# Performance work log

Measured on AMD Instinct MI355X. Metric: run time of the kernel, lower is better.

Reference implementation:

```python
import jax, jax.numpy as jnp
import numpy as np

B, C, F_IN, F_OUT = 2048, 63, 250, 250
NEG_SLOPE = 0.2
N = B * C  # flattened node count


def _build_edge_index():
    # fixed fully-connected (no self) graph over the FIRST 63 nodes only
    src = np.array([i for i in range(C) for j in range(C) if i != j], dtype=np.int32)
    dst = np.array([j for i in range(C) for j in range(C) if i != j], dtype=np.int32)
    # PyG GATConv add_self_loops=True: self loop for every node (num_nodes = N)
    loops = np.arange(N, dtype=np.int32)
    src = np.concatenate([src, loops])
    dst = np.concatenate([dst, loops])
    return jnp.asarray(np.stack([src, dst]))  # [2, E]


def setup_inputs() -> dict:
    key = jax.random.key(0)
    kx, kw, ks, kd = jax.random.split(key, 4)
    x = jax.random.normal(kx, (B, 1, C, F_IN), dtype=jnp.float32)
    # GATConv params (heads=1): lin weight, att_src, att_dst, bias
    W = jax.random.normal(kw, (F_IN, F_OUT), dtype=jnp.float32) / np.sqrt(F_IN)
    att_src = jax.random.normal(ks, (F_OUT,), dtype=jnp.float32) / np.sqrt(F_OUT)
    att_dst = jax.random.normal(kd, (F_OUT,), dtype=jnp.float32) / np.sqrt(F_OUT)
    bias = jnp.zeros((F_OUT,), dtype=jnp.float32)
    return {"x": x, "W": W, "att_src": att_src, "att_dst": att_dst,
            "bias": bias, "edge_index": _build_edge_index()}


def reference(x, W, att_src, att_dst, bias, edge_index):
    b, _, c, f = x.shape
    n = b * c
    h = x.reshape(n, f) @ W                      # [N, F_OUT]
    a_src = h @ att_src                          # [N]
    a_dst = h @ att_dst                          # [N]
    src, dst = edge_index[0], edge_index[1]
    e = jax.nn.leaky_relu(a_src[src] + a_dst[dst], NEG_SLOPE)  # [E]
    # segment softmax over incoming edges of each dst node (stable)
    m = jax.ops.segment_max(e, dst, num_segments=n)
    ex = jnp.exp(e - m[dst])
    denom = jax.ops.segment_sum(ex, dst, num_segments=n)
    alpha = ex / denom[dst]                      # [E]
    out = jax.ops.segment_sum(alpha[:, None] * h[src], dst, num_segments=n)
    out = out + bias
    return out.reshape(b, 1, c, -1)              # [B,1,63,F_OUT]
```

## Files before the change

kernel.cpp:

```cpp
#include <hip/hip_runtime.h>
#include <cstdint>
#include <cstddef>

#define M_TOTAL 129024
#define KDIM    250
#define NDIM    250
#define BM      32
#define TPB     8
#define NBLK    504
#define TILE_F  (BM*KDIM)
#define LDSF    8008

typedef float  f32x4  __attribute__((ext_vector_type(4)));
typedef float  f32x2  __attribute__((ext_vector_type(2)));
typedef __bf16 bf16x8 __attribute__((ext_vector_type(8)));

static __device__ __forceinline__ unsigned short f2bf(float f) {
  unsigned u = __float_as_uint(f);
  u += 0x7fffu + ((u >> 16) & 1u);
  return (unsigned short)(u >> 16);
}

static __device__ __forceinline__ float wsum(float v) {
#pragma unroll
  for (int o = 32; o > 0; o >>= 1) v += __shfl_xor(v, o, 64);
  return v;
}
static __device__ __forceinline__ float wmaxr(float v) {
#pragma unroll
  for (int o = 32; o > 0; o >>= 1) v = fmaxf(v, __shfl_xor(v, o, 64));
  return v;
}

static __device__ __forceinline__ void gll16(const float* g, float* l) {
  __builtin_amdgcn_global_load_lds(
      (const __attribute__((address_space(1))) void*)g,
      (__attribute__((address_space(3))) void*)l, 16, 0, 0);
}
static __device__ __forceinline__ void gll4(const float* g, float* l) {
  __builtin_amdgcn_global_load_lds(
      (const __attribute__((address_space(1))) void*)g,
      (__attribute__((address_space(3))) void*)l, 4, 0, 0);
}

__global__ void wcvt_kernel(const float* __restrict__ W, unsigned short* __restrict__ WTf) {
  const int f     = blockIdx.x * 256 + threadIdx.x;
  const int lane  = f & 63;
  const int kk    = (f >> 6) & 7;
  const int ntile = f >> 9;
  const int n     = ntile * 16 + (lane & 15);
  const int k0    = kk * 32 + (lane >> 4) * 8;
  unsigned u[4];
#pragma unroll
  for (int p = 0; p < 4; ++p) {
    const int ka = k0 + 2 * p, kb = k0 + 2 * p + 1;
    unsigned short a = (n < NDIM && ka < KDIM) ? f2bf(W[(size_t)ka * NDIM + n]) : 0;
    unsigned short b = (n < NDIM && kb < KDIM) ? f2bf(W[(size_t)kb * NDIM + n]) : 0;
    u[p] = (unsigned)a | ((unsigned)b << 16);
  }
  *reinterpret_cast<uint4*>(WTf + (size_t)f * 8) = make_uint4(u[0], u[1], u[2], u[3]);
}

__global__ __launch_bounds__(256, 2) void gemm_kernel(
    const float* __restrict__ X, const unsigned short* __restrict__ WTf,
    const float* __restrict__ bias, float* __restrict__ out,
    float* __restrict__ h63) {
  __shared__ __attribute__((aligned(16))) float lX[2 * LDSF];

  const int tid  = threadIdx.x;
  const int lane = tid & 63;
  const int w    = tid >> 6;
  const int r16  = lane & 15;
  const int quad = lane >> 4;

  if (tid < 8) { lX[TILE_F + tid] = 0.f; lX[LDSF + TILE_F + tid] = 0.f; }

  bf16x8 wf[4][8];
#pragma unroll
  for (int ft = 0; ft < 4; ++ft)
#pragma unroll
    for (int kk = 0; kk < 8; ++kk)
      wf[ft][kk] = *reinterpret_cast<const bf16x8*>(
          WTf + (size_t)((((w * 4 + ft) * 8) + kk) * 64 + lane) * 8);

  float bv[4][4];
#pragma unroll
  for (int ft = 0; ft < 4; ++ft)
#pragma unroll
    for (int i = 0; i < 4; ++i) {
      const int c = w * 64 + ft * 16 + quad * 4 + i;
      bv[ft][i] = (c < NDIM) ? bias[c] : 0.f;
    }

  const int tile0 = blockIdx.x * TPB;

  auto stage = [&](int buf, int g) {
    const float* gb = X + (size_t)g * TILE_F;
    float* lb = &lX[buf * LDSF];
    if (w < 3) {
#pragma unroll
      for (int c = 0; c < 8; ++c) {
        const int ch = w * 8 + c;
        gll16(gb + ch * 256 + lane * 4, lb + ch * 256);
      }
    } else {
#pragma unroll
      for (int c = 0; c < 7; ++c) {
        const int ch = 24 + c;
        gll16(gb + ch * 256 + lane * 4, lb + ch * 256);
      }
      gll4(gb + 7936 + lane, lb + 7936);
    }
  };

  stage(0, tile0);

  for (int t = 0; t < TPB; ++t) {
    const int cur = t & 1;
    __syncthreads();
    if (t + 1 < TPB) stage(cur ^ 1, tile0 + t + 1);

    const float* Bp = &lX[cur * LDSF];
    f32x4 acc[4][2];
#pragma unroll
    for (int ft = 0; ft < 4; ++ft)
#pragma unroll
      for (int nt = 0; nt < 2; ++nt) acc[ft][nt] = f32x4{0.f, 0.f, 0.f, 0.f};

#pragma unroll
    for (int kk = 0; kk < 8; ++kk) {
      bf16x8 xf[2];
#pragma unroll
      for (int nt = 0; nt < 2; ++nt) {
        const float* p = Bp + (size_t)(nt * 16 + r16) * KDIM + kk * 32 + quad * 8;
        const f32x2 a = *reinterpret_cast<const f32x2*>(p);
        const f32x2 b = *reinterpret_cast<const f32x2*>(p + 2);
        const f32x2 c = *reinterpret_cast<const f32x2*>(p + 4);
        const f32x2 d = *reinterpret_cast<const f32x2*>(p + 6);
        bf16x8 v;
        v[0] = (__bf16)a.x; v[1] = (__bf16)a.y;
        v[2] = (__bf16)b.x; v[3] = (__bf16)b.y;
        v[4] = (__bf16)c.x; v[5] = (__bf16)c.y;
        v[6] = (__bf16)d.x; v[7] = (__bf16)d.y;
        xf[nt] = v;
      }
#pragma unroll
      for (int ft = 0; ft < 4; ++ft)
#pragma unroll
        for (int nt = 0; nt < 2; ++nt)
          acc[ft][nt] = __builtin_amdgcn_mfma_f32_16x16x32_bf16(
              wf[ft][kk], xf[nt], acc[ft][nt], 0, 0, 0);
    }

    const int rbase = (tile0 + t) * BM;
#pragma unroll
    for (int ft = 0; ft < 4; ++ft) {
      const int c0 = w * 64 + ft * 16 + quad * 4;
#pragma unroll
      for (int nt = 0; nt < 2; ++nt) {
        const int row = rbase + nt * 16 + r16;
        float* o = out + (size_t)row * NDIM + c0;
        const f32x4 a = acc[ft][nt];
        if (c0 + 1 < NDIM) {
          f32x2 s = {a.x + bv[ft][0], a.y + bv[ft][1]};
          *reinterpret_cast<f32x2*>(o) = s;
        }
        if (c0 + 3 < NDIM) {
          f32x2 s = {a.z + bv[ft][2], a.w + bv[ft][3]};
          *reinterpret_cast<f32x2*>(o + 2) = s;
        }
      }
    }
    if (rbase < 63) {
#pragma unroll
      for (int ft = 0; ft < 4; ++ft) {
        const int c0 = w * 64 + ft * 16 + quad * 4;
#pragma unroll
        for (int nt = 0; nt < 2; ++nt) {
          const int row = rbase + nt * 16 + r16;
          if (row < 63) {
            const f32x4 a = acc[ft][nt];
#pragma unroll
            for (int i = 0; i < 4; ++i)
              if (c0 + i < NDIM) h63[(size_t)row * NDIM + c0 + i] = a[i];
          }
        }
      }
    }
  }
}

__global__ void att_kernel(const float* __restrict__ h, const float* __restrict__ att_src,
                           const float* __restrict__ att_dst, const float* __restrict__ bias,
                           float* __restrict__ out) {
  const int d = blockIdx.x;
  const int tid = threadIdx.x;
  const int lane = tid & 63;
  const int wid = tid >> 6;

  __shared__ float s_asrc[64];
  __shared__ float s_adst;
  __shared__ float s_alpha[64];

  for (int s = wid; s < 63; s += 4) {
    float sum = 0.f;
    for (int f = lane; f < NDIM; f += 64) sum += h[s * NDIM + f] * att_src[f];
    sum = wsum(sum);
    if (lane == 0) s_asrc[s] = sum;
  }
  if (wid == 0) {
    float sum = 0.f;
    for (int f = lane; f < NDIM; f += 64) sum += h[d * NDIM + f] * att_dst[f];
    sum = wsum(sum);
    if (lane == 0) s_adst = sum;
  }
  __syncthreads();

  if (wid == 0) {
    float e = -__builtin_inff();
    if (lane < 63) {
      float x = s_asrc[lane] + s_adst;
      e = (x > 0.f) ? x : 0.2f * x;
    }
    const float m = wmaxr(e);
    const float p = (lane < 63) ? expf(e - m) : 0.f;
    const float den = wsum(p);
    s_alpha[lane] = p / den;
  }
  __syncthreads();

  const int f = tid;
  if (f < NDIM) {
    float o = bias[f];
    for (int s = 0; s < 63; ++s) o += s_alpha[s] * h[s * NDIM + f];
    out[(size_t)d * NDIM + f] = o;
  }
}

extern "C" void kernel_launch(void* const* d_in, const int* in_sizes, int n_in,
                              void* d_out, int out_size, void* d_ws, size_t ws_size,
                              hipStream_t stream) {
  const float* X       = (const float*)d_in[0];
  const float* W       = (const float*)d_in[1];
  const float* att_src = (const float*)d_in[2];
  const float* att_dst = (const float*)d_in[3];
  const float* bias    = (const float*)d_in[4];
  float* out = (float*)d_out;

  unsigned short* WTf = (unsigned short*)d_ws;
  float* h63 = (float*)((char*)d_ws + 131072);

  wcvt_kernel<<<32, 256, 0, stream>>>(W, WTf);
  gemm_kernel<<<NBLK, 256, 0, stream>>>(X, WTf, bias, out, h63);
  att_kernel<<<63, 256, 0, stream>>>(h63, att_src, att_dst, bias, out);
}
```

Measured before the change: 283.2 us.

## Stage GEMM output through LDS for coalesced nontemporal stores, single-buffer input

The GEMM epilogue now writes results into an LDS output tile and then stores it to global memory as contiguous 16-byte nontemporal vectors, replacing the scattered 8-byte row-strided stores. The input X tile becomes single-buffered, so the next tile's load is issued only after compute, overlapping with the output store rather than with the MFMA work. Tiles per block are halved and the grid doubled to keep the GPU filled. The gain is coalesced writes of the large output, at the cost of losing load/compute overlap and adding an extra barrier per tile.

```diff
diff --git a/kernel.cpp b/kernel.cpp
--- a/kernel.cpp
+++ b/kernel.cpp
@@ -6,10 +6,9 @@
 #define KDIM    250
 #define NDIM    250
 #define BM      32
-#define TPB     8
-#define NBLK    504
+#define TPB     4
+#define NBLK    1008
 #define TILE_F  (BM*KDIM)
-#define LDSF    8008
 
 typedef float  f32x4  __attribute__((ext_vector_type(4)));
 typedef float  f32x2  __attribute__((ext_vector_type(2)));
@@ -65,7 +64,8 @@
     const float* __restrict__ X, const unsigned short* __restrict__ WTf,
     const float* __restrict__ bias, float* __restrict__ out,
     float* __restrict__ h63) {
-  __shared__ __attribute__((aligned(16))) float lX[2 * LDSF];
+  __shared__ __attribute__((aligned(16))) float lX[TILE_F + 8];
+  __shared__ __attribute__((aligned(16))) float lO[TILE_F];
 
   const int tid  = threadIdx.x;
   const int lane = tid & 63;
@@ -73,7 +73,7 @@
   const int r16  = lane & 15;
   const int quad = lane >> 4;
 
-  if (tid < 8) { lX[TILE_F + tid] = 0.f; lX[LDSF + TILE_F + tid] = 0.f; }
+  if (tid < 8) lX[TILE_F + tid] = 0.f;
 
   bf16x8 wf[4][8];
 #pragma unroll
@@ -94,33 +94,29 @@
 
   const int tile0 = blockIdx.x * TPB;
 
-  auto stage = [&](int buf, int g) {
+  auto stage = [&](int g) {
     const float* gb = X + (size_t)g * TILE_F;
-    float* lb = &lX[buf * LDSF];
     if (w < 3) {
 #pragma unroll
       for (int c = 0; c < 8; ++c) {
         const int ch = w * 8 + c;
-        gll16(gb + ch * 256 + lane * 4, lb + ch * 256);
+        gll16(gb + ch * 256 + lane * 4, lX + ch * 256);
       }
     } else {
 #pragma unroll
       for (int c = 0; c < 7; ++c) {
         const int ch = 24 + c;
-        gll16(gb + ch * 256 + lane * 4, lb + ch * 256);
-      }
-      gll4(gb + 7936 + lane, lb + 7936);
+        gll16(gb + ch * 256 + lane * 4, lX + ch * 256);
+      }
+      gll4(gb + 7936 + lane, lX + 7936);
     }
   };
 
-  stage(0, tile0);
+  stage(tile0);
 
   for (int t = 0; t < TPB; ++t) {
-    const int cur = t & 1;
     __syncthreads();
-    if (t + 1 < TPB) stage(cur ^ 1, tile0 + t + 1);
-
-    const float* Bp = &lX[cur * LDSF];
+
     f32x4 acc[4][2];
 #pragma unroll
     for (int ft = 0; ft < 4; ++ft)
@@ -132,7 +128,7 @@
       bf16x8 xf[2];
 #pragma unroll
       for (int nt = 0; nt < 2; ++nt) {
-        const float* p = Bp + (size_t)(nt * 16 + r16) * KDIM + kk * 32 + quad * 8;
+        const float* p = lX + (size_t)(nt * 16 + r16) * KDIM + kk * 32 + quad * 8;
         const f32x2 a = *reinterpret_cast<const f32x2*>(p);
         const f32x2 b = *reinterpret_cast<const f32x2*>(p + 2);
         const f32x2 c = *reinterpret_cast<const f32x2*>(p + 4);
@@ -158,16 +154,14 @@
       const int c0 = w * 64 + ft * 16 + quad * 4;
 #pragma unroll
       for (int nt = 0; nt < 2; ++nt) {
-        const int row = rbase + nt * 16 + r16;
-        float* o = out + (size_t)row * NDIM + c0;
+        const int row = nt * 16 + r16;
+        float* o = lO + (size_t)row * KDIM + c0;
         const f32x4 a = acc[ft][nt];
-        if (c0 + 1 < NDIM) {
-          f32x2 s = {a.x + bv[ft][0], a.y + bv[ft][1]};
-          *reinterpret_cast<f32x2*>(o) = s;
-        }
         if (c0 + 3 < NDIM) {
-          f32x2 s = {a.z + bv[ft][2], a.w + bv[ft][3]};
-          *reinterpret_cast<f32x2*>(o + 2) = s;
+          *reinterpret_cast<f32x2*>(o)     = f32x2{a.x + bv[ft][0], a.y + bv[ft][1]};
+          *reinterpret_cast<f32x2*>(o + 2) = f32x2{a.z + bv[ft][2], a.w + bv[ft][3]};
+        } else if (c0 + 1 < NDIM) {
+          *reinterpret_cast<f32x2*>(o) = f32x2{a.x + bv[ft][0], a.y + bv[ft][1]};
         }
       }
     }
@@ -185,6 +179,19 @@
               if (c0 + i < NDIM) h63[(size_t)row * NDIM + c0 + i] = a[i];
           }
         }
+      }
+    }
+
+    __syncthreads();
+    if (t + 1 < TPB) stage(tile0 + t + 1);
+
+    float* ob = out + (size_t)(tile0 + t) * TILE_F;
+#pragma unroll
+    for (int c = 0; c < 8; ++c) {
+      const int flat = c * 1024 + tid * 4;
+      if (c < 7 || tid < 208) {
+        const f32x4 v = *reinterpret_cast<const f32x4*>(lO + flat);
+        __builtin_nontemporal_store(v, reinterpret_cast<f32x4*>(ob + flat));
       }
     }
   }
```

After: 274.1 us. 1.03x faster.
